# Kernel optimization log

Measured on AMD Instinct MI355X. Metric: run time of the kernel, lower is better.

## Reference

```python
import jax, jax.numpy as jnp
import numpy as np

# Model config (matches init_kwargs)
L_F, DELTA_F, L_S, DELTA_S = 1, 1, 32, 16
HIDDEN = 32       # SSM state dim H
GRU_H = 64        # slow-branch GRU hidden
N_GRU = 4
B, T = 4, 32768


def setup_inputs() -> dict:
    key = jax.random.key(0)
    ks = jax.random.split(key, 13)
    def nrm(k, shape, s=0.05):
        return jax.random.normal(k, shape, dtype=jnp.float32) * s
    return {
        "x": jax.random.normal(ks[0], (B, T), dtype=jnp.float32),
        # SlowBranch params
        "fc_in_w": nrm(ks[1], (GRU_H, 1), 0.3),
        "fc_in_b": nrm(ks[2], (GRU_H,)),
        "gru_wih": nrm(ks[3], (N_GRU, 3 * GRU_H, GRU_H), 0.1),
        "gru_whh": nrm(ks[4], (N_GRU, 3 * GRU_H, GRU_H), 0.1),
        "gru_bih": nrm(ks[5], (N_GRU, 3 * GRU_H)),
        "gru_bhh": nrm(ks[6], (N_GRU, 3 * GRU_H)),
        "out_fc_w": nrm(ks[7], (2 * HIDDEN, GRU_H), 0.1),
        "out_fc_b": nrm(ks[8], (2 * HIDDEN,)),
        # Fast branch params (F_IN: 1->H, F_OUT: H->1)
        "fin_w": nrm(ks[9], (HIDDEN, 1), 0.3),
        "fin_b": nrm(ks[10], (HIDDEN,)),
        "fout_w": nrm(ks[11], (1, HIDDEN), 0.1),
        "fout_b": nrm(ks[12], (1,)),
    }


def _gru_layer(xs, Wih, Whh, bih, bhh):
    """Torch-convention GRU layer. xs: (N, L, H_in) -> (N, L, H)."""
    H = Whh.shape[1]
    # Precompute input-side gate pre-activations: (N, L, 3H)
    xp = jnp.einsum('nlh,gh->nlg', xs, Wih) + bih
    def step(h, xt):
        gh = h @ Whh.T + bhh                       # (N, 3H)
        ir, iz, inew = jnp.split(xt, 3, axis=-1)
        hr, hz, hnew = jnp.split(gh, 3, axis=-1)
        r = jax.nn.sigmoid(ir + hr)
        z = jax.nn.sigmoid(iz + hz)
        n = jnp.tanh(inew + r * hnew)
        h = (1.0 - z) * n + z * h
        return h, h
    h0 = jnp.zeros((xs.shape[0], H), xs.dtype)
    _, ys = jax.lax.scan(step, h0, jnp.swapaxes(xp, 0, 1))  # (L, N, H)
    return jnp.swapaxes(ys, 0, 1)


def reference(x, fc_in_w, fc_in_b, gru_wih, gru_whh, gru_bih, gru_bhh,
              out_fc_w, out_fc_b, fin_w, fin_b, fout_w, fout_b):
    Bsz, Tlen = x.shape
    num_slow = (Tlen - L_S) // DELTA_S + 1

    frame_idx = jnp.arange(num_slow)[:, None] * DELTA_S + jnp.arange(L_S)[None, :]
    x_s = x[:, frame_idx].reshape(Bsz * num_slow, L_S, 1)      # (N, L_s, 1)
    h = jax.nn.relu(x_s * fc_in_w[:, 0] + fc_in_b)             # (N, L_s, GRU_H)
    for l in range(gru_wih.shape[0]):
        h = _gru_layer(h, gru_wih[l], gru_whh[l], gru_bih[l], gru_bhh[l])
    eps = h[:, -1, :] @ out_fc_w.T + out_fc_b                  # (N, 2H)
    eps = eps.reshape(Bsz, num_slow, 2 * HIDDEN)
    A_slow = jax.nn.sigmoid(eps[..., :HIDDEN])                 # (B, S, H)
    g_slow = eps[..., HIDDEN:]                                 # (B, S, H)

    # ---- Fast branch: per-sample diagonal linear SSM scan ----
    delta = DELTA_S // DELTA_F
    idx = jnp.clip(jnp.arange(Tlen) // delta - 1, 0, num_slow - 1)  # (T,)
    A_t = A_slow[:, idx, :]                                    # (B, T, H)
    u_t = (x[..., None] * fin_w[:, 0] + fin_b) * g_slow[:, idx, :]  # (B, T, H)

    def step(hc, inp):
        A, u = inp
        hn = A * hc + u
        return hn, hn
    h0 = jnp.zeros((Bsz, HIDDEN), x.dtype)
    _, h_all = jax.lax.scan(step, h0,
                            (jnp.swapaxes(A_t, 0, 1), jnp.swapaxes(u_t, 0, 1)))
    # h_all: (T, B, H); F_OUT applied to every state
    return jnp.einsum('tbh,h->bt', h_all, fout_w[0]) + fout_b[0]   # (B, T)
```

## Files before the change

kernel.cpp:

```cpp
#include <hip/hip_runtime.h>
#include <hip/hip_bf16.h>

typedef __bf16 bf16x8 __attribute__((ext_vector_type(8)));
typedef short short8 __attribute__((ext_vector_type(8)));
typedef float f32x4 __attribute__((ext_vector_type(4)));
typedef unsigned short ushort_t;

#define T_LEN 32768
#define B_SZ 4
#define NSLOW 2047
#define NSEQ (B_SZ * NSLOW)
#define GH 64
#define G3 192
#define NL 4
#define HID 32
#define NCH 256
#define L2E 1.44269504088896341f

static __device__ __forceinline__ float bf2f(ushort_t u) {
    union { unsigned u; float f; } c; c.u = ((unsigned)u) << 16; return c.f;
}
static __device__ __forceinline__ ushort_t f2bf(float f) {
    union { float f; unsigned u; } c; c.f = f;
    unsigned r = (c.u + 0x7FFFu + ((c.u >> 16) & 1u)) >> 16;
    return (ushort_t)r;
}
static __device__ __forceinline__ unsigned pk2bf(float a, float b) {
    float2 f; f.x = a; f.y = b;
    __hip_bfloat162 h = __float22bfloat162_rn(f);
    unsigned u;
    __builtin_memcpy(&u, &h, 4);
    return u;
}
static __device__ __forceinline__ float cvt(float v) { return v; }
static __device__ __forceinline__ float cvt(ushort_t v) { return bf2f(v); }
static __device__ __forceinline__ f32x4 mfma16(short8 a, short8 b, f32x4 c) {
    return __builtin_amdgcn_mfma_f32_16x16x32_bf16(
        __builtin_bit_cast(bf16x8, a), __builtin_bit_cast(bf16x8, b), c, 0, 0, 0);
}
static __device__ __forceinline__ int xoff(int t, int kb, int seq) {
    return ((((t << 3) + kb) << 4) + (seq ^ (kb & 7))) << 3;
}

static __device__ __forceinline__ bool detect_bf16(const void* xin) {
    const ushort_t* xb = (const ushort_t*)xin;
    int lane = threadIdx.x & 63;
    int cnt = 0;
#pragma unroll
    for (int i = 0; i < 4; ++i) {
        ushort_t u = xb[lane * 4 + i];
        int e = (u >> 7) & 0xFF;
        cnt += (e >= 80 && e <= 141) ? 1 : 0;
    }
#pragma unroll
    for (int d = 1; d < 64; d <<= 1) cnt += __shfl_xor(cnt, d, 64);
    return cnt >= 224;
}
static __device__ __forceinline__ float ldf(const void* p, bool isbf, int idx) {
    return isbf ? bf2f(((const ushort_t*)p)[idx]) : ((const float*)p)[idx];
}
static __device__ __forceinline__ short8 load_frag(const void* base, bool isbf,
                                                   int off, float s) {
    short8 o;
    if (isbf) {
        uint4 r = *(const uint4*)((const ushort_t*)base + off);
        unsigned aa[4] = {r.x, r.y, r.z, r.w};
#pragma unroll
        for (int i = 0; i < 4; ++i) {
            o[2 * i]     = (short)f2bf(bf2f((ushort_t)(aa[i] & 0xffffu)) * s);
            o[2 * i + 1] = (short)f2bf(bf2f((ushort_t)(aa[i] >> 16)) * s);
        }
    } else {
        const float4* p = (const float4*)((const float*)base + off);
        float4 a = p[0], b = p[1];
        o[0] = (short)f2bf(a.x * s); o[1] = (short)f2bf(a.y * s);
        o[2] = (short)f2bf(a.z * s); o[3] = (short)f2bf(a.w * s);
        o[4] = (short)f2bf(b.x * s); o[5] = (short)f2bf(b.y * s);
        o[6] = (short)f2bf(b.z * s); o[7] = (short)f2bf(b.w * s);
    }
    return o;
}

template <typename T>
static __device__ __forceinline__ void fill_layer0(
    const T* __restrict__ xT, const T* __restrict__ fcwT,
    const T* __restrict__ fcbT, short8* __restrict__ Xs8, int tid, int n0)
{
    const int seq = tid & 15, kb = (tid >> 4) & 7, tb = tid >> 7;
    int n = n0 + seq; if (n > NSEQ - 1) n = NSEQ - 1;
    int b = n / NSLOW, s = n - b * NSLOW;
    float wv[8], bv[8];
#pragma unroll
    for (int i = 0; i < 8; ++i) {
        wv[i] = cvt(fcwT[kb * 8 + i]);
        bv[i] = cvt(fcbT[kb * 8 + i]);
    }
    const T* xp = xT + b * T_LEN + s * 16;
#pragma unroll
    for (int ii = 0; ii < 16; ++ii) {
        int t = ii * 2 + tb;
        float xv = cvt(xp[t]);
        short8 v;
#pragma unroll
        for (int i = 0; i < 8; ++i) {
            float h = fmaf(xv, wv[i], bv[i]);
            v[i] = (short)f2bf(h > 0.f ? h : 0.f);
        }
        Xs8[xoff(t, kb, seq) >> 3] = v;
    }
}

__global__ __launch_bounds__(256, 2) void gru_kernel(
    const void* __restrict__ xin, const void* __restrict__ fcw,
    const void* __restrict__ fcb, const void* __restrict__ wih,
    const void* __restrict__ whh, const void* __restrict__ bih,
    const void* __restrict__ bhh, const void* __restrict__ ofw,
    const void* __restrict__ ofb, float* __restrict__ Aslow,
    float* __restrict__ gslow)
{
    __shared__ short8 Xs8[4096];
    short* Xs = (short*)Xs8;
    const int tid = threadIdx.x;
    const int w = tid >> 6, lane = tid & 63;
    const int q = lane >> 4, m = lane & 15;
    const int jb = w * 16;
    const int n0 = blockIdx.x * 16;

    const bool isbf = detect_bf16(xin);
    if (isbf)
        fill_layer0((const ushort_t*)xin, (const ushort_t*)fcw,
                    (const ushort_t*)fcb, Xs8, tid, n0);
    else
        fill_layer0((const float*)xin, (const float*)fcw,
                    (const float*)fcb, Xs8, tid, n0);

    const int col0 = jb + 4 * q;
    const int kbw = (col0 >> 3);
    const int wsub = (col0 & 7);
    const int kofs = q * 8;
    const int wbase0 = ((kbw << 4) + (m ^ (kbw & 7))) * 8 + wsub;

    float hc[4];
#pragma unroll 1
    for (int l = 0; l < NL; ++l) {
        const int wl = l * G3 * GH;
        short8 wR0 = load_frag(wih, isbf, wl + (0 * 64 + jb + m) * 64 + kofs, -L2E);
        short8 wR1 = load_frag(wih, isbf, wl + (0 * 64 + jb + m) * 64 + 32 + kofs, -L2E);
        short8 wZ0 = load_frag(wih, isbf, wl + (1 * 64 + jb + m) * 64 + kofs, -L2E);
        short8 wZ1 = load_frag(wih, isbf, wl + (1 * 64 + jb + m) * 64 + 32 + kofs, -L2E);
        short8 wN0 = load_frag(wih, isbf, wl + (2 * 64 + jb + m) * 64 + kofs, 2.f * L2E);
        short8 wN1 = load_frag(wih, isbf, wl + (2 * 64 + jb + m) * 64 + 32 + kofs, 2.f * L2E);
        short8 uR0 = load_frag(whh, isbf, wl + (0 * 64 + jb + m) * 64 + kofs, -L2E);
        short8 uR1 = load_frag(whh, isbf, wl + (0 * 64 + jb + m) * 64 + 32 + kofs, -L2E);
        short8 uZ0 = load_frag(whh, isbf, wl + (1 * 64 + jb + m) * 64 + kofs, -L2E);
        short8 uZ1 = load_frag(whh, isbf, wl + (1 * 64 + jb + m) * 64 + 32 + kofs, -L2E);
        short8 uN0 = load_frag(whh, isbf, wl + (2 * 64 + jb + m) * 64 + kofs, 2.f * L2E);
        short8 uN1 = load_frag(whh, isbf, wl + (2 * 64 + jb + m) * 64 + 32 + kofs, 2.f * L2E);

        f32x4 bRv, bZv, bNXv, bNHv;
#pragma unroll
        for (int i = 0; i < 4; ++i) {
            int c = col0 + i;
            bRv[i]  = -L2E * (ldf(bih, isbf, l * G3 + c) + ldf(bhh, isbf, l * G3 + c));
            bZv[i]  = -L2E * (ldf(bih, isbf, l * G3 + 64 + c) + ldf(bhh, isbf, l * G3 + 64 + c));
            bNXv[i] = 2.f * L2E * ldf(bih, isbf, l * G3 + 128 + c);
            bNHv[i] = 2.f * L2E * ldf(bhh, isbf, l * G3 + 128 + c);
        }

        hc[0] = hc[1] = hc[2] = hc[3] = 0.f;

        __syncthreads();
        int iA = xoff(0, q, m) >> 3;
        int iB = xoff(0, 4 + q, m) >> 3;
        int wb = wbase0;

        short8 cx0 = Xs8[iA], cx1 = Xs8[iB];
        short8 nx0 = Xs8[iA + 128], nx1 = Xs8[iB + 128];
        f32x4 xR = bRv, xZ = bZv, xN = bNXv;
        xR = mfma16(wR0, cx0, xR); xR = mfma16(wR1, cx1, xR);
        xZ = mfma16(wZ0, cx0, xZ); xZ = mfma16(wZ1, cx1, xZ);
        xN = mfma16(wN0, cx0, xN); xN = mfma16(wN1, cx1, xN);
#pragma unroll
        for (int i = 0; i < 4; ++i) {
            float r = __builtin_amdgcn_rcpf(1.f + __builtin_amdgcn_exp2f(xR[i]));
            float z = __builtin_amdgcn_rcpf(1.f + __builtin_amdgcn_exp2f(xZ[i]));
            float yp = fmaf(r, bNHv[i], xN[i]);
            float nn = fmaf(-2.f,
                __builtin_amdgcn_rcpf(1.f + __builtin_amdgcn_exp2f(yp)), 1.f);
            hc[i] = fmaf(z, hc[i] - nn, nn);
        }
        *(uint2*)(Xs + wb) = make_uint2(pk2bf(hc[0], hc[1]), pk2bf(hc[2], hc[3]));
        xR = bRv; xZ = bZv; xN = bNXv;
        xR = mfma16(wR0, nx0, xR); xR = mfma16(wR1, nx1, xR);
        xZ = mfma16(wZ0, nx0, xZ); xZ = mfma16(wZ1, nx1, xZ);
        xN = mfma16(wN0, nx0, xN); xN = mfma16(wN1, nx1, xN);
        iA += 128; iB += 128; wb += 1024;

#pragma unroll 1
        for (int t = 1; t < 32; ++t) {
            __syncthreads();
            short8 bh0 = Xs8[iA - 128];
            short8 bh1 = Xs8[iB - 128];
            short8 px0, px1;
            if (t < 31) {
                px0 = Xs8[iA + 128];
                px1 = Xs8[iB + 128];
            }
            f32x4 aR = xR, aZ = xZ, aNH = bNHv;
            aR  = mfma16(uR0, bh0, aR);  aR  = mfma16(uR1, bh1, aR);
            aZ  = mfma16(uZ0, bh0, aZ);  aZ  = mfma16(uZ1, bh1, aZ);
            aNH = mfma16(uN0, bh0, aNH); aNH = mfma16(uN1, bh1, aNH);
#pragma unroll
            for (int i = 0; i < 4; ++i) {
                float r = __builtin_amdgcn_rcpf(1.f + __builtin_amdgcn_exp2f(aR[i]));
                float z = __builtin_amdgcn_rcpf(1.f + __builtin_amdgcn_exp2f(aZ[i]));
                float yp = fmaf(r, aNH[i], xN[i]);
                float nn = fmaf(-2.f,
                    __builtin_amdgcn_rcpf(1.f + __builtin_amdgcn_exp2f(yp)), 1.f);
                hc[i] = fmaf(z, hc[i] - nn, nn);
            }
            *(uint2*)(Xs + wb) =
                make_uint2(pk2bf(hc[0], hc[1]), pk2bf(hc[2], hc[3]));
            if (t < 31) {
                xR = bRv; xZ = bZv; xN = bNXv;
                xR = mfma16(wR0, px0, xR); xR = mfma16(wR1, px1, xR);
                xZ = mfma16(wZ0, px0, xZ); xZ = mfma16(wZ1, px1, xZ);
                xN = mfma16(wN0, px0, xN); xN = mfma16(wN1, px1, xN);
            }
            iA += 128; iB += 128; wb += 1024;
        }
    }

    __syncthreads();
    short8 aL0 = Xs8[xoff(31, q, m) >> 3];
    short8 aL1 = Xs8[xoff(31, 4 + q, m) >> 3];
    float sc = (w < 2) ? -L2E : 1.f;
    short8 o0 = load_frag(ofw, isbf, (jb + m) * 64 + kofs, sc);
    short8 o1 = load_frag(ofw, isbf, (jb + m) * 64 + 32 + kofs, sc);
    f32x4 aE = {ldf(ofb, isbf, col0) * sc, ldf(ofb, isbf, col0 + 1) * sc,
                ldf(ofb, isbf, col0 + 2) * sc, ldf(ofb, isbf, col0 + 3) * sc};
    aE = mfma16(o0, aL0, aE);
    aE = mfma16(o1, aL1, aE);
    int n = n0 + m;
    if (w < 2) {
        f32x4 v;
#pragma unroll
        for (int i = 0; i < 4; ++i)
            v[i] = __builtin_amdgcn_rcpf(1.f + __builtin_amdgcn_exp2f(aE[i]));
        *(f32x4*)(Aslow + n * HID + col0) = v;
    } else {
        *(f32x4*)(gslow + n * HID + (col0 - 32)) = aE;
    }
}

template <typename T>
static __device__ __forceinline__ void p1_body(
    const T* __restrict__ x, const float* __restrict__ Aslow,
    const float* __restrict__ gslow, const T* __restrict__ finw,
    const T* __restrict__ finb, float* __restrict__ Hpre,
    float* __restrict__ Pl, float* __restrict__ Sl, float* __restrict__ Hl,
    int tid, int bid)
{
    const int b = bid >> 3, h0 = (bid & 7) * 4;
#pragma unroll 1
    for (int p = 0; p < 4; ++p) {
        int idx = p * 256 + tid;
        int lh = idx & 3, c = idx >> 2;
        int h = h0 + lh;
        float fw = cvt(finw[h]), fb = cvt(finb[h]);
        float Pv = 1.f, Sv = 0.f;
        int t0 = c * 128;
#pragma unroll 1
        for (int seg = 0; seg < 8; ++seg) {
            int sidx = c * 8 + seg - 1;
            if (sidx < 0) sidx = 0;
            float A = Aslow[(b * NSLOW + sidx) * HID + h];
            float g = gslow[(b * NSLOW + sidx) * HID + h];
            float fwg = fw * g, fbg = fb * g;
            const T* px = x + b * T_LEN + t0 + seg * 16;
            float xs[16];
#pragma unroll
            for (int j = 0; j < 16; ++j) xs[j] = cvt(px[j]);
#pragma unroll
            for (int j = 0; j < 16; ++j)
                Sv = fmaf(A, Sv, fmaf(xs[j], fwg, fbg));
            float A2 = A * A, A4 = A2 * A2, A8 = A4 * A4;
            Pv *= A8 * A8;
        }
        Pl[c * 4 + lh] = Pv;
        Sl[c * 4 + lh] = Sv;
    }
    __syncthreads();
    if (tid < 4) {
        int lh = tid;
        float hr = 0.f;
#pragma unroll 4
        for (int c = 0; c < NCH; ++c) {
            float pv = Pl[c * 4 + lh], sv = Sl[c * 4 + lh];
            Hl[lh * NCH + c] = hr;
            hr = fmaf(pv, hr, sv);
        }
    }
    __syncthreads();
#pragma unroll 1
    for (int p = 0; p < 4; ++p) {
        int idx = p * 256 + tid;
        int lh = idx >> 8, c = idx & 255;
        Hpre[(b * HID + h0 + lh) * NCH + c] = Hl[lh * NCH + c];
    }
}

__global__ __launch_bounds__(256) void p1scan_kernel(
    const void* __restrict__ xin, const float* __restrict__ Aslow,
    const float* __restrict__ gslow, const void* __restrict__ finw,
    const void* __restrict__ finb, float* __restrict__ Hpre)
{
    __shared__ float Pl[NCH * 4], Sl[NCH * 4], Hl[4 * NCH];
    const bool isbf = detect_bf16(xin);
    if (isbf)
        p1_body((const ushort_t*)xin, Aslow, gslow, (const ushort_t*)finw,
                (const ushort_t*)finb, Hpre, Pl, Sl, Hl, threadIdx.x, blockIdx.x);
    else
        p1_body((const float*)xin, Aslow, gslow, (const float*)finw,
                (const float*)finb, Hpre, Pl, Sl, Hl, threadIdx.x, blockIdx.x);
}

template <typename T>
static __device__ __forceinline__ void pass2_body(
    const T* __restrict__ x, const float* __restrict__ Aslow,
    const float* __restrict__ gslow, const float* __restrict__ Hpre,
    const T* __restrict__ finw, const T* __restrict__ finb,
    const T* __restrict__ fow, const T* __restrict__ fob,
    void* __restrict__ outv, int tid, int bid)
{
    int wv = bid * 4 + (tid >> 6);
    int lane = tid & 63, half = lane >> 5, h = lane & 31;
    int pair = wv * 2 + half;
    int b = pair >> 8, c = pair & 255;
    float hv = Hpre[(b * HID + h) * NCH + c];
    float fw = cvt(finw[h]), fb = cvt(finb[h]);
    float wo = cvt(fow[h]), ob = cvt(fob[0]);
    int t0 = c * 128;
#pragma unroll 1
    for (int blk = 0; blk < 4; ++blk) {
        float ykeep = 0.f;
        float A = 0.f, fwg = 0.f, fbg = 0.f;
#pragma unroll
        for (int tt = 0; tt < 32; ++tt) {
            int t = t0 + blk * 32 + tt;
            if ((tt & 15) == 0) {
                int sidx = (t >> 4) - 1;
                if (sidx < 0) sidx = 0;
                A = Aslow[(b * NSLOW + sidx) * HID + h];
                float g = gslow[(b * NSLOW + sidx) * HID + h];
                fwg = fw * g; fbg = fb * g;
            }
            float xv = cvt(x[b * T_LEN + t]);
            hv = fmaf(A, hv, fmaf(xv, fwg, fbg));
            float y = hv * wo;
            y += __shfl_xor(y, 1, 64);
            y += __shfl_xor(y, 2, 64);
            y += __shfl_xor(y, 4, 64);
            y += __shfl_xor(y, 8, 64);
            y += __shfl_xor(y, 16, 64);
            if (tt == h) ykeep = y + ob;
        }
        int oidx = b * T_LEN + t0 + blk * 32 + h;
        if (sizeof(T) == 2) ((ushort_t*)outv)[oidx] = f2bf(ykeep);
        else                ((float*)outv)[oidx] = ykeep;
    }
}

__global__ __launch_bounds__(256) void pass2_kernel(
    const void* __restrict__ xin, const float* __restrict__ Aslow,
    const float* __restrict__ gslow, const float* __restrict__ Hpre,
    const void* __restrict__ finw, const void* __restrict__ finb,
    const void* __restrict__ fow, const void* __restrict__ fob,
    void* __restrict__ outv)
{
    const bool isbf = detect_bf16(xin);
    if (isbf)
        pass2_body((const ushort_t*)xin, Aslow, gslow, Hpre,
                   (const ushort_t*)finw, (const ushort_t*)finb,
                   (const ushort_t*)fow, (const ushort_t*)fob,
                   outv, threadIdx.x, blockIdx.x);
    else
        pass2_body((const float*)xin, Aslow, gslow, Hpre,
                   (const float*)finw, (const float*)finb,
                   (const float*)fow, (const float*)fob,
                   outv, threadIdx.x, blockIdx.x);
}

extern "C" void kernel_launch(void* const* d_in, const int* in_sizes, int n_in,
                              void* d_out, int out_size, void* d_ws, size_t ws_size,
                              hipStream_t stream)
{
    const void* xin  = d_in[0];
    const void* fcw  = d_in[1];
    const void* fcb  = d_in[2];
    const void* wih  = d_in[3];
    const void* whh  = d_in[4];
    const void* bih  = d_in[5];
    const void* bhh  = d_in[6];
    const void* ofw  = d_in[7];
    const void* ofb  = d_in[8];
    const void* finw = d_in[9];
    const void* finb = d_in[10];
    const void* fow  = d_in[11];
    const void* fob  = d_in[12];

    float* Aslow = (float*)d_ws;
    float* gslow = Aslow + 8192 * 32;
    float* Hpre  = gslow + 8192 * 32;

    gru_kernel<<<dim3(512), dim3(256), 0, stream>>>(
        xin, fcw, fcb, wih, whh, bih, bhh, ofw, ofb, Aslow, gslow);
    p1scan_kernel<<<dim3(32), dim3(256), 0, stream>>>(
        xin, Aslow, gslow, finw, finb, Hpre);
    pass2_kernel<<<dim3(128), dim3(256), 0, stream>>>(
        xin, Aslow, gslow, Hpre, finw, finb, fow, fob, d_out);
}
```

Before: 195.1 us.

## Split GRU waves into input-projection producers and recurrent consumers

The GRU kernel now launches 512 threads per block. Four waves compute the input-side gate projections one timestep ahead and hand them over through a double-buffered fp16 LDS buffer. The other four waves run only the recurrent matmul and the gate math, so the input projection is taken off the serial critical path. In exchange the handoff values are rounded to fp16, each step pays extra LDS traffic and a block-wide barrier, and dynamic shared memory use grows to about 82KB, which may cut the number of resident blocks per CU.

After: 205.9 us. 5.6% more time.

```diff
diff --git a/kernel.cpp b/kernel.cpp
--- a/kernel.cpp
+++ b/kernel.cpp
@@ -17,6 +17,11 @@
 #define NCH 256
 #define L2E 1.44269504088896341f
 
+#define XB_STRIDE 72
+#define XB_GATE  (16 * XB_STRIDE)
+#define XB_PP    (3 * XB_GATE)
+#define GRU_LDS  (65536 + 2 * XB_PP * 2)
+
 static __device__ __forceinline__ float bf2f(ushort_t u) {
     union { unsigned u; float f; } c; c.u = ((unsigned)u) << 16; return c.f;
 }
@@ -31,6 +36,13 @@
     unsigned u;
     __builtin_memcpy(&u, &h, 4);
     return u;
+}
+static __device__ __forceinline__ ushort_t f16b(float f) {
+    _Float16 h = (_Float16)f;
+    ushort_t u; __builtin_memcpy(&u, &h, 2); return u;
+}
+static __device__ __forceinline__ float f16f(ushort_t u) {
+    _Float16 h; __builtin_memcpy(&h, &u, 2); return (float)h;
 }
 static __device__ __forceinline__ float cvt(float v) { return v; }
 static __device__ __forceinline__ float cvt(ushort_t v) { return bf2f(v); }
@@ -86,7 +98,8 @@
     const T* __restrict__ xT, const T* __restrict__ fcwT,
     const T* __restrict__ fcbT, short8* __restrict__ Xs8, int tid, int n0)
 {
-    const int seq = tid & 15, kb = (tid >> 4) & 7, tb = tid >> 7;
+    const int seq = tid & 15, kb = (tid >> 4) & 7;
+    const int tb = tid >> 7;
     int n = n0 + seq; if (n > NSEQ - 1) n = NSEQ - 1;
     int b = n / NSLOW, s = n - b * NSLOW;
     float wv[8], bv[8];
@@ -97,8 +110,8 @@
     }
     const T* xp = xT + b * T_LEN + s * 16;
 #pragma unroll
-    for (int ii = 0; ii < 16; ++ii) {
-        int t = ii * 2 + tb;
+    for (int ii = 0; ii < 8; ++ii) {
+        int t = ii * 4 + tb;
         float xv = cvt(xp[t]);
         short8 v;
 #pragma unroll
@@ -110,7 +123,7 @@
     }
 }
 
-__global__ __launch_bounds__(256, 2) void gru_kernel(
+__global__ __launch_bounds__(512, 4) void gru_kernel(
     const void* __restrict__ xin, const void* __restrict__ fcw,
     const void* __restrict__ fcb, const void* __restrict__ wih,
     const void* __restrict__ whh, const void* __restrict__ bih,
@@ -118,12 +131,14 @@
     const void* __restrict__ ofb, float* __restrict__ Aslow,
     float* __restrict__ gslow)
 {
-    __shared__ short8 Xs8[4096];
-    short* Xs = (short*)Xs8;
+    extern __shared__ short Xs[];
+    short8* Xs8 = (short8*)Xs;
+    ushort_t* xb = (ushort_t*)(Xs + 32768);
     const int tid = threadIdx.x;
     const int w = tid >> 6, lane = tid & 63;
     const int q = lane >> 4, m = lane & 15;
-    const int jb = w * 16;
+    const int p = w & 3, jb = p * 16;
+    const bool isG = (w < 4);
     const int n0 = blockIdx.x * 16;
 
     const bool isbf = detect_bf16(xin);
@@ -139,117 +154,134 @@
     const int wsub = (col0 & 7);
     const int kofs = q * 8;
     const int wbase0 = ((kbw << 4) + (m ^ (kbw & 7))) * 8 + wsub;
+    const int xbo = m * XB_STRIDE + col0;
+    const int iA = xoff(0, q, m) >> 3;
+    const int iB = xoff(0, 4 + q, m) >> 3;
 
     float hc[4];
 #pragma unroll 1
     for (int l = 0; l < NL; ++l) {
         const int wl = l * G3 * GH;
-        short8 wR0 = load_frag(wih, isbf, wl + (0 * 64 + jb + m) * 64 + kofs, -L2E);
-        short8 wR1 = load_frag(wih, isbf, wl + (0 * 64 + jb + m) * 64 + 32 + kofs, -L2E);
-        short8 wZ0 = load_frag(wih, isbf, wl + (1 * 64 + jb + m) * 64 + kofs, -L2E);
-        short8 wZ1 = load_frag(wih, isbf, wl + (1 * 64 + jb + m) * 64 + 32 + kofs, -L2E);
-        short8 wN0 = load_frag(wih, isbf, wl + (2 * 64 + jb + m) * 64 + kofs, 2.f * L2E);
-        short8 wN1 = load_frag(wih, isbf, wl + (2 * 64 + jb + m) * 64 + 32 + kofs, 2.f * L2E);
-        short8 uR0 = load_frag(whh, isbf, wl + (0 * 64 + jb + m) * 64 + kofs, -L2E);
-        short8 uR1 = load_frag(whh, isbf, wl + (0 * 64 + jb + m) * 64 + 32 + kofs, -L2E);
-        short8 uZ0 = load_frag(whh, isbf, wl + (1 * 64 + jb + m) * 64 + kofs, -L2E);
-        short8 uZ1 = load_frag(whh, isbf, wl + (1 * 64 + jb + m) * 64 + 32 + kofs, -L2E);
-        short8 uN0 = load_frag(whh, isbf, wl + (2 * 64 + jb + m) * 64 + kofs, 2.f * L2E);
-        short8 uN1 = load_frag(whh, isbf, wl + (2 * 64 + jb + m) * 64 + 32 + kofs, 2.f * L2E);
-
-        f32x4 bRv, bZv, bNXv, bNHv;
-#pragma unroll
-        for (int i = 0; i < 4; ++i) {
-            int c = col0 + i;
-            bRv[i]  = -L2E * (ldf(bih, isbf, l * G3 + c) + ldf(bhh, isbf, l * G3 + c));
-            bZv[i]  = -L2E * (ldf(bih, isbf, l * G3 + 64 + c) + ldf(bhh, isbf, l * G3 + 64 + c));
-            bNXv[i] = 2.f * L2E * ldf(bih, isbf, l * G3 + 128 + c);
-            bNHv[i] = 2.f * L2E * ldf(bhh, isbf, l * G3 + 128 + c);
-        }
-
+        short8 f0, f1, f2, f3, f4, f5;
+        f32x4 cR, cZ, cN;
+        if (isG) {
+            f0 = load_frag(whh, isbf, wl + (0 * 64 + jb + m) * 64 + kofs, -L2E);
+            f1 = load_frag(whh, isbf, wl + (0 * 64 + jb + m) * 64 + 32 + kofs, -L2E);
+            f2 = load_frag(whh, isbf, wl + (1 * 64 + jb + m) * 64 + kofs, -L2E);
+            f3 = load_frag(whh, isbf, wl + (1 * 64 + jb + m) * 64 + 32 + kofs, -L2E);
+            f4 = load_frag(whh, isbf, wl + (2 * 64 + jb + m) * 64 + kofs, 2.f * L2E);
+            f5 = load_frag(whh, isbf, wl + (2 * 64 + jb + m) * 64 + 32 + kofs, 2.f * L2E);
+#pragma unroll
+            for (int i = 0; i < 4; ++i)
+                cN[i] = 2.f * L2E * ldf(bhh, isbf, l * G3 + 128 + col0 + i);
+        } else {
+            f0 = load_frag(wih, isbf, wl + (0 * 64 + jb + m) * 64 + kofs, -L2E);
+            f1 = load_frag(wih, isbf, wl + (0 * 64 + jb + m) * 64 + 32 + kofs, -L2E);
+            f2 = load_frag(wih, isbf, wl + (1 * 64 + jb + m) * 64 + kofs, -L2E);
+            f3 = load_frag(wih, isbf, wl + (1 * 64 + jb + m) * 64 + 32 + kofs, -L2E);
+            f4 = load_frag(wih, isbf, wl + (2 * 64 + jb + m) * 64 + kofs, 2.f * L2E);
+            f5 = load_frag(wih, isbf, wl + (2 * 64 + jb + m) * 64 + 32 + kofs, 2.f * L2E);
+#pragma unroll
+            for (int i = 0; i < 4; ++i) {
+                int c = col0 + i;
+                cR[i] = -L2E * (ldf(bih, isbf, l * G3 + c) + ldf(bhh, isbf, l * G3 + c));
+                cZ[i] = -L2E * (ldf(bih, isbf, l * G3 + 64 + c) + ldf(bhh, isbf, l * G3 + 64 + c));
+                cN[i] = 2.f * L2E * ldf(bih, isbf, l * G3 + 128 + c);
+            }
+        }
         hc[0] = hc[1] = hc[2] = hc[3] = 0.f;
 
         __syncthreads();
-        int iA = xoff(0, q, m) >> 3;
-        int iB = xoff(0, 4 + q, m) >> 3;
-        int wb = wbase0;
-
-        short8 cx0 = Xs8[iA], cx1 = Xs8[iB];
-        short8 nx0 = Xs8[iA + 128], nx1 = Xs8[iB + 128];
-        f32x4 xR = bRv, xZ = bZv, xN = bNXv;
-        xR = mfma16(wR0, cx0, xR); xR = mfma16(wR1, cx1, xR);
-        xZ = mfma16(wZ0, cx0, xZ); xZ = mfma16(wZ1, cx1, xZ);
-        xN = mfma16(wN0, cx0, xN); xN = mfma16(wN1, cx1, xN);
-#pragma unroll
-        for (int i = 0; i < 4; ++i) {
-            float r = __builtin_amdgcn_rcpf(1.f + __builtin_amdgcn_exp2f(xR[i]));
-            float z = __builtin_amdgcn_rcpf(1.f + __builtin_amdgcn_exp2f(xZ[i]));
-            float yp = fmaf(r, bNHv[i], xN[i]);
-            float nn = fmaf(-2.f,
-                __builtin_amdgcn_rcpf(1.f + __builtin_amdgcn_exp2f(yp)), 1.f);
-            hc[i] = fmaf(z, hc[i] - nn, nn);
-        }
-        *(uint2*)(Xs + wb) = make_uint2(pk2bf(hc[0], hc[1]), pk2bf(hc[2], hc[3]));
-        xR = bRv; xZ = bZv; xN = bNXv;
-        xR = mfma16(wR0, nx0, xR); xR = mfma16(wR1, nx1, xR);
-        xZ = mfma16(wZ0, nx0, xZ); xZ = mfma16(wZ1, nx1, xZ);
-        xN = mfma16(wN0, nx0, xN); xN = mfma16(wN1, nx1, xN);
-        iA += 128; iB += 128; wb += 1024;
-
-#pragma unroll 1
-        for (int t = 1; t < 32; ++t) {
+        if (!isG) {
+            short8 x0 = Xs8[iA], x1 = Xs8[iB];
+            f32x4 xR = cR, xZ = cZ, xN = cN;
+            xR = mfma16(f0, x0, xR); xR = mfma16(f1, x1, xR);
+            xZ = mfma16(f2, x0, xZ); xZ = mfma16(f3, x1, xZ);
+            xN = mfma16(f4, x0, xN); xN = mfma16(f5, x1, xN);
+            f32x4 acc3[3] = {xR, xZ, xN};
+#pragma unroll
+            for (int g = 0; g < 3; ++g) {
+                uint2 v;
+                v.x = f16b(acc3[g][0]) | ((unsigned)f16b(acc3[g][1]) << 16);
+                v.y = f16b(acc3[g][2]) | ((unsigned)f16b(acc3[g][3]) << 16);
+                *(uint2*)(xb + g * XB_GATE + xbo) = v;
+            }
+        }
+        __syncthreads();
+
+#pragma unroll 1
+        for (int t = 0; t < 32; ++t) {
+            if (isG) {
+                int xo = (t & 1) * XB_PP + xbo;
+                uint2 vR = *(const uint2*)(xb + xo);
+                uint2 vZ = *(const uint2*)(xb + xo + XB_GATE);
+                uint2 vN = *(const uint2*)(xb + xo + 2 * XB_GATE);
+                f32x4 aR  = {f16f((ushort_t)vR.x), f16f((ushort_t)(vR.x >> 16)),
+                             f16f((ushort_t)vR.y), f16f((ushort_t)(vR.y >> 16))};
+                f32x4 aZ  = {f16f((ushort_t)vZ.x), f16f((ushort_t)(vZ.x >> 16)),
+                             f16f((ushort_t)vZ.y), f16f((ushort_t)(vZ.y >> 16))};
+                f32x4 aNX = {f16f((ushort_t)vN.x), f16f((ushort_t)(vN.x >> 16)),
+                             f16f((ushort_t)vN.y), f16f((ushort_t)(vN.y >> 16))};
+                f32x4 aNH = cN;
+                if (t > 0) {
+                    short8 bh0 = Xs8[iA + (t - 1) * 128];
+                    short8 bh1 = Xs8[iB + (t - 1) * 128];
+                    aR  = mfma16(f0, bh0, aR);  aR  = mfma16(f1, bh1, aR);
+                    aZ  = mfma16(f2, bh0, aZ);  aZ  = mfma16(f3, bh1, aZ);
+                    aNH = mfma16(f4, bh0, aNH); aNH = mfma16(f5, bh1, aNH);
+                }
+#pragma unroll
+                for (int i = 0; i < 4; ++i) {
+                    float r = __builtin_amdgcn_rcpf(1.f + __builtin_amdgcn_exp2f(aR[i]));
+                    float z = __builtin_amdgcn_rcpf(1.f + __builtin_amdgcn_exp2f(aZ[i]));
+                    float yp = fmaf(r, aNH[i], aNX[i]);
+                    float nn = fmaf(-2.f,
+                        __builtin_amdgcn_rcpf(1.f + __builtin_amdgcn_exp2f(yp)), 1.f);
+                    hc[i] = fmaf(z, hc[i] - nn, nn);
+                }
+                *(uint2*)(Xs + wbase0 + t * 1024) =
+                    make_uint2(pk2bf(hc[0], hc[1]), pk2bf(hc[2], hc[3]));
+            } else if (t < 31) {
+                short8 x0 = Xs8[iA + (t + 1) * 128];
+                short8 x1 = Xs8[iB + (t + 1) * 128];
+                f32x4 xR = cR, xZ = cZ, xN = cN;
+                xR = mfma16(f0, x0, xR); xR = mfma16(f1, x1, xR);
+                xZ = mfma16(f2, x0, xZ); xZ = mfma16(f3, x1, xZ);
+                xN = mfma16(f4, x0, xN); xN = mfma16(f5, x1, xN);
+                f32x4 acc3[3] = {xR, xZ, xN};
+                int xo = ((t + 1) & 1) * XB_PP + xbo;
+#pragma unroll
+                for (int g = 0; g < 3; ++g) {
+                    uint2 v;
+                    v.x = f16b(acc3[g][0]) | ((unsigned)f16b(acc3[g][1]) << 16);
+                    v.y = f16b(acc3[g][2]) | ((unsigned)f16b(acc3[g][3]) << 16);
+                    *(uint2*)(xb + xo + g * XB_GATE) = v;
+                }
+            }
             __syncthreads();
-            short8 bh0 = Xs8[iA - 128];
-            short8 bh1 = Xs8[iB - 128];
-            short8 px0, px1;
-            if (t < 31) {
-                px0 = Xs8[iA + 128];
-                px1 = Xs8[iB + 128];
-            }
-            f32x4 aR = xR, aZ = xZ, aNH = bNHv;
-            aR  = mfma16(uR0, bh0, aR);  aR  = mfma16(uR1, bh1, aR);
-            aZ  = mfma16(uZ0, bh0, aZ);  aZ  = mfma16(uZ1, bh1, aZ);
-            aNH = mfma16(uN0, bh0, aNH); aNH = mfma16(uN1, bh1, aNH);
-#pragma unroll
-            for (int i = 0; i < 4; ++i) {
-                float r = __builtin_amdgcn_rcpf(1.f + __builtin_amdgcn_exp2f(aR[i]));
-                float z = __builtin_amdgcn_rcpf(1.f + __builtin_amdgcn_exp2f(aZ[i]));
-                float yp = fmaf(r, aNH[i], xN[i]);
-                float nn = fmaf(-2.f,
-                    __builtin_amdgcn_rcpf(1.f + __builtin_amdgcn_exp2f(yp)), 1.f);
-                hc[i] = fmaf(z, hc[i] - nn, nn);
-            }
-            *(uint2*)(Xs + wb) =
-                make_uint2(pk2bf(hc[0], hc[1]), pk2bf(hc[2], hc[3]));
-            if (t < 31) {
-                xR = bRv; xZ = bZv; xN = bNXv;
-                xR = mfma16(wR0, px0, xR); xR = mfma16(wR1, px1, xR);
-                xZ = mfma16(wZ0, px0, xZ); xZ = mfma16(wZ1, px1, xZ);
-                xN = mfma16(wN0, px0, xN); xN = mfma16(wN1, px1, xN);
-            }
-            iA += 128; iB += 128; wb += 1024;
-        }
-    }
-
-    __syncthreads();
-    short8 aL0 = Xs8[xoff(31, q, m) >> 3];
-    short8 aL1 = Xs8[xoff(31, 4 + q, m) >> 3];
-    float sc = (w < 2) ? -L2E : 1.f;
-    short8 o0 = load_frag(ofw, isbf, (jb + m) * 64 + kofs, sc);
-    short8 o1 = load_frag(ofw, isbf, (jb + m) * 64 + 32 + kofs, sc);
-    f32x4 aE = {ldf(ofb, isbf, col0) * sc, ldf(ofb, isbf, col0 + 1) * sc,
-                ldf(ofb, isbf, col0 + 2) * sc, ldf(ofb, isbf, col0 + 3) * sc};
-    aE = mfma16(o0, aL0, aE);
-    aE = mfma16(o1, aL1, aE);
-    int n = n0 + m;
-    if (w < 2) {
-        f32x4 v;
-#pragma unroll
-        for (int i = 0; i < 4; ++i)
-            v[i] = __builtin_amdgcn_rcpf(1.f + __builtin_amdgcn_exp2f(aE[i]));
-        *(f32x4*)(Aslow + n * HID + col0) = v;
-    } else {
-        *(f32x4*)(gslow + n * HID + (col0 - 32)) = aE;
+        }
+    }
+
+    if (isG) {
+        short8 aL0 = Xs8[iA + 31 * 128];
+        short8 aL1 = Xs8[iB + 31 * 128];
+        float sc = (w < 2) ? -L2E : 1.f;
+        short8 o0 = load_frag(ofw, isbf, (jb + m) * 64 + kofs, sc);
+        short8 o1 = load_frag(ofw, isbf, (jb + m) * 64 + 32 + kofs, sc);
+        f32x4 aE = {ldf(ofb, isbf, col0) * sc, ldf(ofb, isbf, col0 + 1) * sc,
+                    ldf(ofb, isbf, col0 + 2) * sc, ldf(ofb, isbf, col0 + 3) * sc};
+        aE = mfma16(o0, aL0, aE);
+        aE = mfma16(o1, aL1, aE);
+        int n = n0 + m;
+        if (w < 2) {
+            f32x4 v;
+#pragma unroll
+            for (int i = 0; i < 4; ++i)
+                v[i] = __builtin_amdgcn_rcpf(1.f + __builtin_amdgcn_exp2f(aE[i]));
+            *(f32x4*)(Aslow + n * HID + col0) = v;
+        } else {
+            *(f32x4*)(gslow + n * HID + (col0 - 32)) = aE;
+        }
     }
 }
 
@@ -413,7 +445,10 @@
     float* gslow = Aslow + 8192 * 32;
     float* Hpre  = gslow + 8192 * 32;
 
-    gru_kernel<<<dim3(512), dim3(256), 0, stream>>>(
+    hipFuncSetAttribute((const void*)gru_kernel,
+                        hipFuncAttributeMaxDynamicSharedMemorySize, GRU_LDS);
+
+    gru_kernel<<<dim3(512), dim3(512), GRU_LDS, stream>>>(
         xin, fcw, fcb, wih, whh, bih, bhh, ofw, ofb, Aslow, gslow);
     p1scan_kernel<<<dim3(32), dim3(256), 0, stream>>>(
         xin, Aslow, gslow, finw, finb, Hpre);
```

## Wavefront-pipeline the four GRU layers across warps in one block

Applied to the files above, without the earlier changes.

The GRU kernel now runs all four layers at once in a 1024-thread block: each group of four warps owns one layer and processes time step t=c-l, giving a diagonal wavefront over 35 stages instead of 4x32 serial steps. Hidden states pass between layers through a ring buffer of four time slots per layer in shared memory. The layer-0 input projection (fc_in + ReLU) is computed on the fly rather than prefilled. This shortens the serial dependency chain and raises parallelism per block, but each stage does the input projection on the critical path, uses a larger block that may cut occupancy, and relies on the 4-slot ring plus one barrier per stage being enough to keep layers in step.

Result: slower. 233.5 us (+19.7%).

```diff
diff --git a/kernel.cpp b/kernel.cpp
--- a/kernel.cpp
+++ b/kernel.cpp
@@ -38,9 +38,6 @@
     return __builtin_amdgcn_mfma_f32_16x16x32_bf16(
         __builtin_bit_cast(bf16x8, a), __builtin_bit_cast(bf16x8, b), c, 0, 0, 0);
 }
-static __device__ __forceinline__ int xoff(int t, int kb, int seq) {
-    return ((((t << 3) + kb) << 4) + (seq ^ (kb & 7))) << 3;
-}
 
 static __device__ __forceinline__ bool detect_bf16(const void* xin) {
     const ushort_t* xb = (const ushort_t*)xin;
@@ -81,36 +78,7 @@
     return o;
 }
 
-template <typename T>
-static __device__ __forceinline__ void fill_layer0(
-    const T* __restrict__ xT, const T* __restrict__ fcwT,
-    const T* __restrict__ fcbT, short8* __restrict__ Xs8, int tid, int n0)
-{
-    const int seq = tid & 15, kb = (tid >> 4) & 7, tb = tid >> 7;
-    int n = n0 + seq; if (n > NSEQ - 1) n = NSEQ - 1;
-    int b = n / NSLOW, s = n - b * NSLOW;
-    float wv[8], bv[8];
-#pragma unroll
-    for (int i = 0; i < 8; ++i) {
-        wv[i] = cvt(fcwT[kb * 8 + i]);
-        bv[i] = cvt(fcbT[kb * 8 + i]);
-    }
-    const T* xp = xT + b * T_LEN + s * 16;
-#pragma unroll
-    for (int ii = 0; ii < 16; ++ii) {
-        int t = ii * 2 + tb;
-        float xv = cvt(xp[t]);
-        short8 v;
-#pragma unroll
-        for (int i = 0; i < 8; ++i) {
-            float h = fmaf(xv, wv[i], bv[i]);
-            v[i] = (short)f2bf(h > 0.f ? h : 0.f);
-        }
-        Xs8[xoff(t, kb, seq) >> 3] = v;
-    }
-}
-
-__global__ __launch_bounds__(256, 2) void gru_kernel(
+__global__ __launch_bounds__(1024, 4) void gru_kernel(
     const void* __restrict__ xin, const void* __restrict__ fcw,
     const void* __restrict__ fcb, const void* __restrict__ wih,
     const void* __restrict__ whh, const void* __restrict__ bih,
@@ -118,138 +86,131 @@
     const void* __restrict__ ofb, float* __restrict__ Aslow,
     float* __restrict__ gslow)
 {
-    __shared__ short8 Xs8[4096];
-    short* Xs = (short*)Xs8;
+    __shared__ short Xs[16384];
     const int tid = threadIdx.x;
     const int w = tid >> 6, lane = tid & 63;
     const int q = lane >> 4, m = lane & 15;
-    const int jb = w * 16;
+    const int l = w >> 2, p = w & 3, jb = p * 16;
     const int n0 = blockIdx.x * 16;
 
     const bool isbf = detect_bf16(xin);
-    if (isbf)
-        fill_layer0((const ushort_t*)xin, (const ushort_t*)fcw,
-                    (const ushort_t*)fcb, Xs8, tid, n0);
-    else
-        fill_layer0((const float*)xin, (const float*)fcw,
-                    (const float*)fcb, Xs8, tid, n0);
 
     const int col0 = jb + 4 * q;
-    const int kbw = (col0 >> 3);
-    const int wsub = (col0 & 7);
+    const int kbw = col0 >> 3, wsub = col0 & 7;
     const int kofs = q * 8;
-    const int wbase0 = ((kbw << 4) + (m ^ (kbw & 7))) * 8 + wsub;
-
-    float hc[4];
-#pragma unroll 1
-    for (int l = 0; l < NL; ++l) {
-        const int wl = l * G3 * GH;
-        short8 wR0 = load_frag(wih, isbf, wl + (0 * 64 + jb + m) * 64 + kofs, -L2E);
-        short8 wR1 = load_frag(wih, isbf, wl + (0 * 64 + jb + m) * 64 + 32 + kofs, -L2E);
-        short8 wZ0 = load_frag(wih, isbf, wl + (1 * 64 + jb + m) * 64 + kofs, -L2E);
-        short8 wZ1 = load_frag(wih, isbf, wl + (1 * 64 + jb + m) * 64 + 32 + kofs, -L2E);
-        short8 wN0 = load_frag(wih, isbf, wl + (2 * 64 + jb + m) * 64 + kofs, 2.f * L2E);
-        short8 wN1 = load_frag(wih, isbf, wl + (2 * 64 + jb + m) * 64 + 32 + kofs, 2.f * L2E);
-        short8 uR0 = load_frag(whh, isbf, wl + (0 * 64 + jb + m) * 64 + kofs, -L2E);
-        short8 uR1 = load_frag(whh, isbf, wl + (0 * 64 + jb + m) * 64 + 32 + kofs, -L2E);
-        short8 uZ0 = load_frag(whh, isbf, wl + (1 * 64 + jb + m) * 64 + kofs, -L2E);
-        short8 uZ1 = load_frag(whh, isbf, wl + (1 * 64 + jb + m) * 64 + 32 + kofs, -L2E);
-        short8 uN0 = load_frag(whh, isbf, wl + (2 * 64 + jb + m) * 64 + kofs, 2.f * L2E);
-        short8 uN1 = load_frag(whh, isbf, wl + (2 * 64 + jb + m) * 64 + 32 + kofs, 2.f * L2E);
-
-        f32x4 bRv, bZv, bNXv, bNHv;
+    const int wbase = ((kbw << 4) + (m ^ (kbw & 7))) * 8 + wsub;
+    const int oA = ((q << 4) + (m ^ q)) << 3;
+    const int oB = (((4 + q) << 4) + (m ^ (4 + q))) << 3;
+    const int rl = l << 12;
+    const int rp = (l - 1) << 12;
+
+    const int wl = l * G3 * GH;
+    short8 wR0 = load_frag(wih, isbf, wl + (0 * 64 + jb + m) * 64 + kofs, -L2E);
+    short8 wR1 = load_frag(wih, isbf, wl + (0 * 64 + jb + m) * 64 + 32 + kofs, -L2E);
+    short8 wZ0 = load_frag(wih, isbf, wl + (1 * 64 + jb + m) * 64 + kofs, -L2E);
+    short8 wZ1 = load_frag(wih, isbf, wl + (1 * 64 + jb + m) * 64 + 32 + kofs, -L2E);
+    short8 wN0 = load_frag(wih, isbf, wl + (2 * 64 + jb + m) * 64 + kofs, 2.f * L2E);
+    short8 wN1 = load_frag(wih, isbf, wl + (2 * 64 + jb + m) * 64 + 32 + kofs, 2.f * L2E);
+    short8 uR0 = load_frag(whh, isbf, wl + (0 * 64 + jb + m) * 64 + kofs, -L2E);
+    short8 uR1 = load_frag(whh, isbf, wl + (0 * 64 + jb + m) * 64 + 32 + kofs, -L2E);
+    short8 uZ0 = load_frag(whh, isbf, wl + (1 * 64 + jb + m) * 64 + kofs, -L2E);
+    short8 uZ1 = load_frag(whh, isbf, wl + (1 * 64 + jb + m) * 64 + 32 + kofs, -L2E);
+    short8 uN0 = load_frag(whh, isbf, wl + (2 * 64 + jb + m) * 64 + kofs, 2.f * L2E);
+    short8 uN1 = load_frag(whh, isbf, wl + (2 * 64 + jb + m) * 64 + 32 + kofs, 2.f * L2E);
+
+    f32x4 bRv, bZv, bNXv, bNHv;
+#pragma unroll
+    for (int i = 0; i < 4; ++i) {
+        int c = col0 + i;
+        bRv[i]  = -L2E * (ldf(bih, isbf, l * G3 + c) + ldf(bhh, isbf, l * G3 + c));
+        bZv[i]  = -L2E * (ldf(bih, isbf, l * G3 + 64 + c) + ldf(bhh, isbf, l * G3 + 64 + c));
+        bNXv[i] = 2.f * L2E * ldf(bih, isbf, l * G3 + 128 + c);
+        bNHv[i] = 2.f * L2E * ldf(bhh, isbf, l * G3 + 128 + c);
+    }
+
+    int n = n0 + m; if (n > NSEQ - 1) n = NSEQ - 1;
+    const int bb = n / NSLOW, ss = n - bb * NSLOW;
+    const int xbase = bb * T_LEN + ss * 16;
+    short8 fw0, fb0, fw1, fb1;
+    if (l == 0) {
+#pragma unroll
+        for (int i = 0; i < 8; ++i) {
+            fw0[i] = (short)f2bf(ldf(fcw, isbf, kofs + i));
+            fb0[i] = (short)f2bf(ldf(fcb, isbf, kofs + i));
+            fw1[i] = (short)f2bf(ldf(fcw, isbf, 32 + kofs + i));
+            fb1[i] = (short)f2bf(ldf(fcb, isbf, 32 + kofs + i));
+        }
+    }
+
+    float hc[4] = {0.f, 0.f, 0.f, 0.f};
+
+#pragma unroll 1
+    for (int c = 0; c < NL - 1 + 32; ++c) {
+        __syncthreads();
+        const int t = c - l;
+        if (t < 0 || t > 31) continue;
+        short8 bx0, bx1;
+        if (l == 0) {
+            float xv = ldf(xin, isbf, xbase + t);
+#pragma unroll
+            for (int i = 0; i < 8; ++i) {
+                float h0 = fmaf(xv, bf2f((ushort_t)fw0[i]), bf2f((ushort_t)fb0[i]));
+                float h1 = fmaf(xv, bf2f((ushort_t)fw1[i]), bf2f((ushort_t)fb1[i]));
+                bx0[i] = (short)f2bf(h0 > 0.f ? h0 : 0.f);
+                bx1[i] = (short)f2bf(h1 > 0.f ? h1 : 0.f);
+            }
+        } else {
+            const int so = (t & 3) << 10;
+            bx0 = *(const short8*)(Xs + rp + so + oA);
+            bx1 = *(const short8*)(Xs + rp + so + oB);
+        }
+        f32x4 aR = bRv, aZ = bZv, aNX = bNXv, aNH = bNHv;
+        aR  = mfma16(wR0, bx0, aR);  aR  = mfma16(wR1, bx1, aR);
+        aZ  = mfma16(wZ0, bx0, aZ);  aZ  = mfma16(wZ1, bx1, aZ);
+        aNX = mfma16(wN0, bx0, aNX); aNX = mfma16(wN1, bx1, aNX);
+        if (t > 0) {
+            const int so = ((t - 1) & 3) << 10;
+            short8 bh0 = *(const short8*)(Xs + rl + so + oA);
+            short8 bh1 = *(const short8*)(Xs + rl + so + oB);
+            aR  = mfma16(uR0, bh0, aR);  aR  = mfma16(uR1, bh1, aR);
+            aZ  = mfma16(uZ0, bh0, aZ);  aZ  = mfma16(uZ1, bh1, aZ);
+            aNH = mfma16(uN0, bh0, aNH); aNH = mfma16(uN1, bh1, aNH);
+        }
 #pragma unroll
         for (int i = 0; i < 4; ++i) {
-            int c = col0 + i;
-            bRv[i]  = -L2E * (ldf(bih, isbf, l * G3 + c) + ldf(bhh, isbf, l * G3 + c));
-            bZv[i]  = -L2E * (ldf(bih, isbf, l * G3 + 64 + c) + ldf(bhh, isbf, l * G3 + 64 + c));
-            bNXv[i] = 2.f * L2E * ldf(bih, isbf, l * G3 + 128 + c);
-            bNHv[i] = 2.f * L2E * ldf(bhh, isbf, l * G3 + 128 + c);
-        }
-
-        hc[0] = hc[1] = hc[2] = hc[3] = 0.f;
-
-        __syncthreads();
-        int iA = xoff(0, q, m) >> 3;
-        int iB = xoff(0, 4 + q, m) >> 3;
-        int wb = wbase0;
-
-        short8 cx0 = Xs8[iA], cx1 = Xs8[iB];
-        short8 nx0 = Xs8[iA + 128], nx1 = Xs8[iB + 128];
-        f32x4 xR = bRv, xZ = bZv, xN = bNXv;
-        xR = mfma16(wR0, cx0, xR); xR = mfma16(wR1, cx1, xR);
-        xZ = mfma16(wZ0, cx0, xZ); xZ = mfma16(wZ1, cx1, xZ);
-        xN = mfma16(wN0, cx0, xN); xN = mfma16(wN1, cx1, xN);
-#pragma unroll
-        for (int i = 0; i < 4; ++i) {
-            float r = __builtin_amdgcn_rcpf(1.f + __builtin_amdgcn_exp2f(xR[i]));
-            float z = __builtin_amdgcn_rcpf(1.f + __builtin_amdgcn_exp2f(xZ[i]));
-            float yp = fmaf(r, bNHv[i], xN[i]);
+            float r = __builtin_amdgcn_rcpf(1.f + __builtin_amdgcn_exp2f(aR[i]));
+            float z = __builtin_amdgcn_rcpf(1.f + __builtin_amdgcn_exp2f(aZ[i]));
+            float yp = fmaf(r, aNH[i], aNX[i]);
             float nn = fmaf(-2.f,
                 __builtin_amdgcn_rcpf(1.f + __builtin_amdgcn_exp2f(yp)), 1.f);
             hc[i] = fmaf(z, hc[i] - nn, nn);
         }
-        *(uint2*)(Xs + wb) = make_uint2(pk2bf(hc[0], hc[1]), pk2bf(hc[2], hc[3]));
-        xR = bRv; xZ = bZv; xN = bNXv;
-        xR = mfma16(wR0, nx0, xR); xR = mfma16(wR1, nx1, xR);
-        xZ = mfma16(wZ0, nx0, xZ); xZ = mfma16(wZ1, nx1, xZ);
-        xN = mfma16(wN0, nx0, xN); xN = mfma16(wN1, nx1, xN);
-        iA += 128; iB += 128; wb += 1024;
-
-#pragma unroll 1
-        for (int t = 1; t < 32; ++t) {
-            __syncthreads();
-            short8 bh0 = Xs8[iA - 128];
-            short8 bh1 = Xs8[iB - 128];
-            short8 px0, px1;
-            if (t < 31) {
-                px0 = Xs8[iA + 128];
-                px1 = Xs8[iB + 128];
-            }
-            f32x4 aR = xR, aZ = xZ, aNH = bNHv;
-            aR  = mfma16(uR0, bh0, aR);  aR  = mfma16(uR1, bh1, aR);
-            aZ  = mfma16(uZ0, bh0, aZ);  aZ  = mfma16(uZ1, bh1, aZ);
-            aNH = mfma16(uN0, bh0, aNH); aNH = mfma16(uN1, bh1, aNH);
-#pragma unroll
-            for (int i = 0; i < 4; ++i) {
-                float r = __builtin_amdgcn_rcpf(1.f + __builtin_amdgcn_exp2f(aR[i]));
-                float z = __builtin_amdgcn_rcpf(1.f + __builtin_amdgcn_exp2f(aZ[i]));
-                float yp = fmaf(r, aNH[i], xN[i]);
-                float nn = fmaf(-2.f,
-                    __builtin_amdgcn_rcpf(1.f + __builtin_amdgcn_exp2f(yp)), 1.f);
-                hc[i] = fmaf(z, hc[i] - nn, nn);
-            }
-            *(uint2*)(Xs + wb) =
-                make_uint2(pk2bf(hc[0], hc[1]), pk2bf(hc[2], hc[3]));
-            if (t < 31) {
-                xR = bRv; xZ = bZv; xN = bNXv;
-                xR = mfma16(wR0, px0, xR); xR = mfma16(wR1, px1, xR);
-                xZ = mfma16(wZ0, px0, xZ); xZ = mfma16(wZ1, px1, xZ);
-                xN = mfma16(wN0, px0, xN); xN = mfma16(wN1, px1, xN);
-            }
-            iA += 128; iB += 128; wb += 1024;
-        }
+        *(uint2*)(Xs + rl + ((t & 3) << 10) + wbase) =
+            make_uint2(pk2bf(hc[0], hc[1]), pk2bf(hc[2], hc[3]));
     }
 
     __syncthreads();
-    short8 aL0 = Xs8[xoff(31, q, m) >> 3];
-    short8 aL1 = Xs8[xoff(31, 4 + q, m) >> 3];
-    float sc = (w < 2) ? -L2E : 1.f;
-    short8 o0 = load_frag(ofw, isbf, (jb + m) * 64 + kofs, sc);
-    short8 o1 = load_frag(ofw, isbf, (jb + m) * 64 + 32 + kofs, sc);
-    f32x4 aE = {ldf(ofb, isbf, col0) * sc, ldf(ofb, isbf, col0 + 1) * sc,
-                ldf(ofb, isbf, col0 + 2) * sc, ldf(ofb, isbf, col0 + 3) * sc};
-    aE = mfma16(o0, aL0, aE);
-    aE = mfma16(o1, aL1, aE);
-    int n = n0 + m;
-    if (w < 2) {
-        f32x4 v;
-#pragma unroll
-        for (int i = 0; i < 4; ++i)
-            v[i] = __builtin_amdgcn_rcpf(1.f + __builtin_amdgcn_exp2f(aE[i]));
-        *(f32x4*)(Aslow + n * HID + col0) = v;
-    } else {
-        *(f32x4*)(gslow + n * HID + (col0 - 32)) = aE;
+    if (l == 3) {
+        const int so = (3 << 12) + ((31 & 3) << 10);
+        short8 aL0 = *(const short8*)(Xs + so + oA);
+        short8 aL1 = *(const short8*)(Xs + so + oB);
+        float sc = (p < 2) ? -L2E : 1.f;
+        short8 o0 = load_frag(ofw, isbf, (jb + m) * 64 + kofs, sc);
+        short8 o1 = load_frag(ofw, isbf, (jb + m) * 64 + 32 + kofs, sc);
+        f32x4 aE = {ldf(ofb, isbf, col0) * sc, ldf(ofb, isbf, col0 + 1) * sc,
+                    ldf(ofb, isbf, col0 + 2) * sc, ldf(ofb, isbf, col0 + 3) * sc};
+        aE = mfma16(o0, aL0, aE);
+        aE = mfma16(o1, aL1, aE);
+        int nn2 = n0 + m;
+        if (p < 2) {
+            f32x4 v;
+#pragma unroll
+            for (int i = 0; i < 4; ++i)
+                v[i] = __builtin_amdgcn_rcpf(1.f + __builtin_amdgcn_exp2f(aE[i]));
+            *(f32x4*)(Aslow + nn2 * HID + col0) = v;
+        } else {
+            *(f32x4*)(gslow + nn2 * HID + (col0 - 32)) = aE;
+        }
     }
 }
 
@@ -413,7 +374,7 @@
     float* gslow = Aslow + 8192 * 32;
     float* Hpre  = gslow + 8192 * 32;
 
-    gru_kernel<<<dim3(512), dim3(256), 0, stream>>>(
+    gru_kernel<<<dim3(512), dim3(1024), 0, stream>>>(
         xin, fcw, fcb, wih, whh, bih, bhh, ofw, ofb, Aslow, gslow);
     p1scan_kernel<<<dim3(32), dim3(256), 0, stream>>>(
         xin, Aslow, gslow, finw, finb, Hpre);
```
